# Kernel tuning notes

Hardware: AMD Instinct MI355X
Metric: run time of the kernel (lower is better)

Reference implementation:

```python
import jax, jax.numpy as jnp
import numpy as np
from jax import lax

T = 36          # sequence length
N_POLES = 80    # N -> dictionary has 2N+1 = 161 atoms
LAM = 0.1       # lam_f
MAX_ITER = 100
TOL = 1e-05


def real_D(T, rho, theta):
    # CONSTR=True: squash rho into [0.001, 1.15], theta into [0, pi]
    rmin, rmax = 0.001, 1.15
    r = rmin + (rmax - rmin) * jax.nn.sigmoid(rho)          # (N,)
    th = jnp.pi * jax.nn.sigmoid(theta)                     # (N,)
    i = jnp.arange(T, dtype=rho.dtype)[:, None]             # (T,1)
    p = r[None, :] ** i                                     # (T,N)
    W1 = p * jnp.cos(i * th[None, :])
    W2 = p * jnp.sin(i * th[None, :])
    D = jnp.concatenate([jnp.ones((T, 1), rho.dtype), W1, W2], axis=1)  # (T, 2N+1)
    # NORM=True: column-normalize all but the constant column
    norms = jnp.linalg.norm(D[:, 1:], axis=0, keepdims=True)
    return jnp.concatenate([D[:, :1], D[:, 1:] / norms], axis=1)


def softshrink(v, thr):
    return jnp.sign(v) * jnp.maximum(jnp.abs(v) - thr, 0.0)


def fista_efc(D, Y, lam, max_iter):
    # argmin_C ||Y - D C||_2^2 + lam |C|_1
    DtD = D.T @ D                                           # (P,P)
    L_inv = 1.0 / jnp.linalg.norm(DtD, ord=2)               # 1/spectral norm
    P = DtD.shape[0]
    dim_data = Y.shape[-1]
    A = jnp.eye(P, dtype=Y.dtype) - L_inv * DtD             # (P,P)
    B = L_inv * jnp.einsum('tp,btd->bpd', D, Y)             # (B,P,d)
    thr = lax.stop_gradient(lam * L_inv)                    # .item() in torch => constant

    batch = Y.shape[0]
    x0 = jnp.zeros((batch, P, dim_data), Y.dtype)
    y0 = jnp.zeros((batch, P, dim_data), Y.dtype)

    def body(carry, _):
        x, y, t, done = carry
        x_new = softshrink(jnp.einsum('pq,bqd->bpd', A, y) + B, thr)
        diff = jnp.linalg.norm(x - x_new) / dim_data        # Frobenius over all elems
        t_new = (1.0 + jnp.sqrt(1.0 + 4.0 * t * t)) / 2.0
        tt = (t - 1.0) / t_new
        y_new = (1.0 + tt) * x_new - tt * x
        # if already converged before this step, freeze the state (early return)
        x_out = jnp.where(done, x, x_new)
        y_out = jnp.where(done, y, y_new)
        t_out = jnp.where(done, t, t_new)
        done_new = done | (diff < TOL)
        return (x_out, y_out, t_out, done_new), None

    init = (x0, y0, jnp.float32(1.0), jnp.bool_(False))
    (x_fin, _, _, _), _ = lax.scan(body, init, None, length=max_iter)
    return x_fin


def reference(x, rho, theta):
    # DAN.forward with wiRH=False, freezeD=False
    dic = real_D(T, rho, theta)                             # (T, 2N+1)
    C = fista_efc(dic, x, LAM, MAX_ITER)                    # (B, 2N+1, d)
    reconst = jnp.einsum('tp,bpd->btd', dic, C)             # (B, T, d)
    return C, dic, reconst


def setup_inputs() -> dict:
    key = jax.random.key(0)
    k1, k2, k3 = jax.random.split(key, 3)
    x = jax.random.normal(k1, (256, T, 50), dtype=jnp.float32)
    rho = jax.random.uniform(k2, (N_POLES,), dtype=jnp.float32)
    theta = jax.random.uniform(k3, (N_POLES,), dtype=jnp.float32)
    return {"x": x, "rho": rho, "theta": theta}
```

## Files before the change

kernel.cpp:

```cpp
#include <hip/hip_runtime.h>
#include <math.h>

typedef _Float16 half_t;
typedef __attribute__((ext_vector_type(8))) _Float16 half8;
typedef __attribute__((ext_vector_type(4))) _Float16 half4;
typedef __attribute__((ext_vector_type(4))) float floatx4;

#define TDIM 36
#define PDIM 161
#define NCOL 50
#define NITER 100
#define PITER8 50

#define NKA 6
#define GSTR 44
#define SPS 196

#define YROW 384
#define RROW 128

#define SWZ(row, byteoff) ((byteoff) ^ (((row) & 7) << 4))

#define BY_Y    0
#define BY_R    24576
#define BY_LRTH 28672
#define BY_SC   32768
#define BY_GS   32784
#define BY_G2   39120
#define BY_G4   45456
#define LDS_TOTAL 51792

#define MFMA16 __builtin_amdgcn_mfma_f32_16x16x32_f16

__global__ __launch_bounds__(768, 3)
void dan_kernel(const float* __restrict__ xin, const float* __restrict__ rho,
                const float* __restrict__ theta, float* __restrict__ outC,
                float* __restrict__ outDic, float* __restrict__ outR)
{
  extern __shared__ char smc[];
  float*  sc   = (float*)(smc + BY_SC);
  float*  Gs   = (float*)(smc + BY_GS);
  float*  G2   = (float*)(smc + BY_G2);
  float*  G4   = (float*)(smc + BY_G4);
  float*  Df   = (float*)(smc + BY_Y);
  float*  lrth = (float*)(smc + BY_LRTH);

  const int tid = threadIdx.x;
  const int b = blockIdx.x;
  const int wave = tid >> 6, lane = tid & 63;
  const int q = lane >> 4, ln = lane & 15;

  {
    unsigned int* z = (unsigned int*)smc;
    for (int i = tid; i < LDS_TOTAL / 4; i += 768) z[i] = 0u;
  }
  __syncthreads();

  if (tid >= 1 && tid < PDIM) {
    const bool is_sin = tid > 80;
    const int n = is_sin ? (tid - 81) : (tid - 1);
    lrth[tid]       = logf(0.001f + 1.149f / (1.0f + expf(-rho[n])));
    lrth[161 + tid] = 3.14159265358979f / (1.0f + expf(-theta[n]));
  }
  __syncthreads();

  for (int i = tid; i < TDIM * PDIM; i += 768) {
    const int t = i / PDIM, p = i - t * PDIM;
    float val;
    if (p == 0) {
      val = 1.0f;
    } else {
      const float ft = (float)t;
      const float e = expf(ft * lrth[p]);
      const float ang = ft * lrth[161 + p];
      val = e * (p > 80 ? sinf(ang) : cosf(ang));
    }
    Df[t * SPS + p] = val;
  }
  __syncthreads();

  if (tid >= 1 && tid < PDIM) {
    float s2 = 0.0f;
    for (int t = 0; t < TDIM; ++t) {
      const float v = Df[t * SPS + tid];
      s2 += v * v;
    }
    const float inv = 1.0f / sqrtf(s2);
    for (int t = 0; t < TDIM; ++t) Df[t * SPS + tid] *= inv;
  }
  __syncthreads();

  if (tid < 666) {
    int i = 0, rem = tid;
    while (rem >= TDIM - i) { rem -= TDIM - i; ++i; }
    const int j = i + rem;
    const float4* ri = (const float4*)(Df + i * SPS);
    const float4* rj = (const float4*)(Df + j * SPS);
    float a = 0.0f;
    #pragma unroll 7
    for (int k = 0; k < SPS / 4; ++k) {
      const float4 x = ri[k], y = rj[k];
      a += x.x * y.x + x.y * y.y + x.z * y.z + x.w * y.w;
    }
    Gs[i * GSTR + j] = a;
    Gs[j * GSTR + i] = a;
  }
  if (b == 0) {
    for (int i = tid; i < TDIM * PDIM; i += 768) {
      const int t = i / PDIM, p = i - t * PDIM;
      outDic[i] = Df[t * SPS + p];
    }
  }

  const int mtA = wave >> 2;
  const int ntA = wave & 3;
  const int g = wave >> 1;
  const int h = wave & 1;

  half8 DhF[NKA], DlF[NKA];
  {
    const int row = 16 * mtA + ln;
    #pragma unroll
    for (int ks = 0; ks < NKA; ++ks) {
      half8 hh = {0,0,0,0,0,0,0,0}, ll = {0,0,0,0,0,0,0,0};
      if (row < TDIM) {
        const float4 f0 = *(const float4*)(Df + row * SPS + 32 * ks + 8 * q);
        const float4 f1 = *(const float4*)(Df + row * SPS + 32 * ks + 8 * q + 4);
        const float fa[8] = {f0.x, f0.y, f0.z, f0.w, f1.x, f1.y, f1.z, f1.w};
        #pragma unroll
        for (int e = 0; e < 8; ++e) {
          const half_t h2 = (half_t)fa[e];
          hh[e] = h2;
          ll[e] = (half_t)(fa[e] - (float)h2);
        }
      }
      DhF[ks] = hh;
      DlF[ks] = ll;
    }
  }
  half8 DtH[2][2];
  #pragma unroll
  for (int k = 0; k < 2; ++k) {
    const int atom = 16 * (g + 6 * k) + ln;
    #pragma unroll
    for (int ks = 0; ks < 2; ++ks) {
      half8 hh;
      #pragma unroll
      for (int e = 0; e < 8; ++e) {
        const int t = 32 * ks + 8 * q + e;
        const float v = (t < TDIM) ? Df[t * SPS + atom] : 0.0f;
        hh[e] = (half_t)v;
      }
      DtH[k][ks] = hh;
    }
  }
  float yA[4];
  {
    const float* xb = xin + b * TDIM * NCOL;
    const int c = 16 * ntA + ln;
    #pragma unroll
    for (int r = 0; r < 4; ++r) {
      const int t = 16 * mtA + 4 * q + r;
      yA[r] = (t < TDIM && c < NCOL) ? xb[t * NCOL + c] : 0.0f;
    }
  }
  __syncthreads();

  if (tid < 666) {
    int i = 0, rem = tid;
    while (rem >= TDIM - i) { rem -= TDIM - i; ++i; }
    const int j = i + rem;
    const float4* ri = (const float4*)(Gs + i * GSTR);
    const float4* rj = (const float4*)(Gs + j * GSTR);
    float a = 0.0f;
    #pragma unroll
    for (int k = 0; k < GSTR / 4; ++k) {
      const float4 x = ri[k], y = rj[k];
      a += x.x * y.x + x.y * y.y + x.z * y.z + x.w * y.w;
    }
    G2[i * GSTR + j] = a;
    G2[j * GSTR + i] = a;
  }
  __syncthreads();
  if (tid < 666) {
    int i = 0, rem = tid;
    while (rem >= TDIM - i) { rem -= TDIM - i; ++i; }
    const int j = i + rem;
    const float4* ri = (const float4*)(G2 + i * GSTR);
    const float4* rj = (const float4*)(G2 + j * GSTR);
    float a = 0.0f;
    #pragma unroll
    for (int k = 0; k < GSTR / 4; ++k) {
      const float4 x = ri[k], y = rj[k];
      a += x.x * y.x + x.y * y.y + x.z * y.z + x.w * y.w;
    }
    G4[i * GSTR + j] = a;
    G4[j * GSTR + i] = a;
  }
  __syncthreads();
  if (tid < 666) {
    int i = 0, rem = tid;
    while (rem >= TDIM - i) { rem -= TDIM - i; ++i; }
    const int j = i + rem;
    const float4* ri = (const float4*)(G4 + i * GSTR);
    const float4* rj = (const float4*)(G4 + j * GSTR);
    float a = 0.0f;
    #pragma unroll
    for (int k = 0; k < GSTR / 4; ++k) {
      const float4 x = ri[k], y = rj[k];
      a += x.x * y.x + x.y * y.y + x.z * y.z + x.w * y.w;
    }
    G2[i * GSTR + j] = a;
    G2[j * GSTR + i] = a;
  }
  __syncthreads();

  if (wave == 0) {
    float g8r[36];
    #pragma unroll
    for (int j = 0; j < 36; ++j) g8r[j] = (lane < 36) ? G2[lane * GSTR + j] : 0.0f;
    float v = (lane < 36) ? 1.0f : 0.0f;
    for (int it = 0; it < PITER8; ++it) {
      const int vi = __float_as_int(v);
      float w0 = 0.0f, w1 = 0.0f, w2 = 0.0f, w3 = 0.0f;
      #pragma unroll
      for (int j = 0; j < 36; j += 4) {
        w0 = fmaf(g8r[j],     __int_as_float(__builtin_amdgcn_readlane(vi, j)),     w0);
        w1 = fmaf(g8r[j + 1], __int_as_float(__builtin_amdgcn_readlane(vi, j + 1)), w1);
        w2 = fmaf(g8r[j + 2], __int_as_float(__builtin_amdgcn_readlane(vi, j + 2)), w2);
        w3 = fmaf(g8r[j + 3], __int_as_float(__builtin_amdgcn_readlane(vi, j + 3)), w3);
      }
      float w = (w0 + w1) + (w2 + w3);
      float s = w * w;
      #pragma unroll
      for (int off = 32; off > 0; off >>= 1) s += __shfl_xor(s, off, 64);
      v = w * rsqrtf(s);
    }
    const int vi = __float_as_int(v);
    float w0 = 0.0f, w1 = 0.0f;
    #pragma unroll
    for (int j = 0; j < 36; j += 2) {
      const float gi0 = (lane < 36) ? Gs[lane * GSTR + j]     : 0.0f;
      const float gi1 = (lane < 36) ? Gs[lane * GSTR + j + 1] : 0.0f;
      w0 = fmaf(gi0, __int_as_float(__builtin_amdgcn_readlane(vi, j)),     w0);
      w1 = fmaf(gi1, __int_as_float(__builtin_amdgcn_readlane(vi, j + 1)), w1);
    }
    float num = v * (w0 + w1);
    #pragma unroll
    for (int off = 32; off > 0; off >>= 1) num += __shfl_xor(num, off, 64);
    if (lane == 0) {
      sc[0] = 1.0f / num;
      sc[1] = 0.1f / num;
    }
  } else {
    unsigned int* z = (unsigned int*)smc;
    for (int i = tid - 64; i < 32768 / 4; i += 704) z[i] = 0u;
  }
  __syncthreads();
  const float L_inv = sc[0];
  const float thr = sc[1];

  float xR[2][2][4], yR[2][2][4];
  #pragma unroll
  for (int k = 0; k < 2; ++k)
    #pragma unroll
    for (int s = 0; s < 2; ++s)
      #pragma unroll
      for (int r = 0; r < 4; ++r) { xR[k][s][r] = 0.0f; yR[k][s][r] = 0.0f; }

  float tk = 1.0f;

  for (int it = 0; it < NITER; ++it) {
    {
      floatx4 aH0 = {0.f,0.f,0.f,0.f}, aH1 = {0.f,0.f,0.f,0.f};
      floatx4 aL0 = {0.f,0.f,0.f,0.f}, aL1 = {0.f,0.f,0.f,0.f};
      const int n0 = 16 * ntA + ln;
      const char* yrow = smc + BY_Y + n0 * YROW;
      #pragma unroll
      for (int ks = 0; ks < NKA; ++ks) {
        const int kb = (32 * ks + 8 * q) * 2;
        const half8 b0 = *(const half8*)(yrow + SWZ(n0, kb));
        if (ks & 1) {
          aH1 = MFMA16(DhF[ks], b0, aH1, 0, 0, 0);
          aL1 = MFMA16(DlF[ks], b0, aL1, 0, 0, 0);
        } else {
          aH0 = MFMA16(DhF[ks], b0, aH0, 0, 0, 0);
          aL0 = MFMA16(DlF[ks], b0, aL0, 0, 0, 0);
        }
      }
      const int t0 = 16 * mtA + 4 * q;
      half4 hv;
      #pragma unroll
      for (int r = 0; r < 4; ++r)
        hv[r] = (half_t)(yA[r] - ((aH0[r] + aH1[r]) + (aL0[r] + aL1[r])));
      *(half4*)(smc + BY_R + n0 * RROW + SWZ(n0, t0 * 2)) = hv;
    }
    __syncthreads();

    const float tnew = 0.5f * (1.0f + sqrtf(1.0f + 4.0f * tk * tk));
    const float ttf = (tk - 1.0f) / tnew;
    tk = tnew;

    {
      half8 rb[2][2];
      #pragma unroll
      for (int s = 0; s < 2; ++s) {
        const int cS = 16 * (2 * h + s) + ln;
        const char* rrow = smc + BY_R + cS * RROW;
        rb[s][0] = *(const half8*)(rrow + SWZ(cS, 16 * q));
        rb[s][1] = *(const half8*)(rrow + SWZ(cS, 64 + 16 * q));
      }

      #pragma unroll
      for (int k = 0; k < 2; ++k) {
        const int pt = g + 6 * k;
        const int p0 = 16 * pt + 4 * q;
        #pragma unroll
        for (int s = 0; s < 2; ++s) {
          floatx4 a = {0.f,0.f,0.f,0.f};
          a = MFMA16(DtH[k][0], rb[s][0], a, 0, 0, 0);
          a = MFMA16(DtH[k][1], rb[s][1], a, 0, 0, 0);
          const int cS = 16 * (2 * h + s) + ln;
          half4 hv;
          #pragma unroll
          for (int r = 0; r < 4; ++r) {
            const float w = yR[k][s][r] + L_inv * a[r];
            const float cl = fminf(fmaxf(w, -thr), thr);
            const float xn = w - cl;
            const float yn = xn + ttf * (xn - xR[k][s][r]);
            xR[k][s][r] = xn;
            yR[k][s][r] = yn;
            hv[r] = (half_t)yn;
          }
          *(half4*)(smc + BY_Y + cS * YROW + SWZ(cS, p0 * 2)) = hv;
        }
      }
    }
    __syncthreads();
  }

  float* Cb = outC + b * PDIM * NCOL;
  #pragma unroll
  for (int k = 0; k < 2; ++k) {
    const int pt = g + 6 * k;
    #pragma unroll
    for (int s = 0; s < 2; ++s) {
      const int cS = 16 * (2 * h + s) + ln;
      if (cS < NCOL) {
        #pragma unroll
        for (int r = 0; r < 4; ++r) {
          const int p = 16 * pt + 4 * q + r;
          if (p < PDIM) Cb[p * NCOL + cS] = xR[k][s][r];
        }
      }
    }
  }
  #pragma unroll
  for (int k = 0; k < 2; ++k) {
    const int pt = g + 6 * k;
    const int p0 = 16 * pt + 4 * q;
    #pragma unroll
    for (int s = 0; s < 2; ++s) {
      const int cS = 16 * (2 * h + s) + ln;
      half4 hv;
      #pragma unroll
      for (int r = 0; r < 4; ++r) hv[r] = (half_t)xR[k][s][r];
      *(half4*)(smc + BY_Y + cS * YROW + SWZ(cS, p0 * 2)) = hv;
    }
  }
  __syncthreads();
  {
    floatx4 aH0 = {0.f,0.f,0.f,0.f}, aH1 = {0.f,0.f,0.f,0.f};
    floatx4 aL0 = {0.f,0.f,0.f,0.f}, aL1 = {0.f,0.f,0.f,0.f};
    const int n0 = 16 * ntA + ln;
    const char* yrow = smc + BY_Y + n0 * YROW;
    #pragma unroll
    for (int ks = 0; ks < NKA; ++ks) {
      const int kb = (32 * ks + 8 * q) * 2;
      const half8 b0 = *(const half8*)(yrow + SWZ(n0, kb));
      if (ks & 1) {
        aH1 = MFMA16(DhF[ks], b0, aH1, 0, 0, 0);
        aL1 = MFMA16(DlF[ks], b0, aL1, 0, 0, 0);
      } else {
        aH0 = MFMA16(DhF[ks], b0, aH0, 0, 0, 0);
        aL0 = MFMA16(DlF[ks], b0, aL0, 0, 0, 0);
      }
    }
    float* Rb = outR + b * TDIM * NCOL;
    const int c = n0;
    if (c < NCOL) {
      const int t0 = 16 * mtA + 4 * q;
      #pragma unroll
      for (int r = 0; r < 4; ++r) {
        const int t = t0 + r;
        if (t < TDIM)
          Rb[t * NCOL + c] = (aH0[r] + aH1[r]) + (aL0[r] + aL1[r]);
      }
    }
  }
}


extern "C" void kernel_launch(void* const* d_in, const int* in_sizes, int n_in,
                              void* d_out, int out_size, void* d_ws, size_t ws_size,
                              hipStream_t stream) {
  const float* x     = (const float*)d_in[0];
  const float* rho   = (const float*)d_in[1];
  const float* theta = (const float*)d_in[2];

  float* out    = (float*)d_out;
  float* outC   = out;
  float* outDic = out + 256 * PDIM * NCOL;
  float* outR   = outDic + TDIM * PDIM;

  hipLaunchKernelGGL(dan_kernel, dim3(256), dim3(768), LDS_TOTAL, stream,
                     x, rho, theta, outC, outDic, outR);
}
```

Measured before the change: 210.9 us.

## Split each batch's 50 columns across two 384-thread blocks

Launches 512 blocks of 384 threads instead of 256 blocks of 768, with each block handling 25 of the 50 data columns of one batch element. The FISTA iterations are independent per column, so this halves per-block work and LDS use and gives more blocks to spread across CUs. The cost is that every block recomputes the dictionary, the Gram powers and the spectral-norm estimate. Column tiles stay 32 wide, so part of the MFMA work on 25 columns is padding.

```diff
diff --git a/kernel.cpp b/kernel.cpp
--- a/kernel.cpp
+++ b/kernel.cpp
@@ -9,6 +9,7 @@
 #define TDIM 36
 #define PDIM 161
 #define NCOL 50
+#define DHALF 25
 #define NITER 100
 #define PITER8 50
 
@@ -22,17 +23,18 @@
 #define SWZ(row, byteoff) ((byteoff) ^ (((row) & 7) << 4))
 
 #define BY_Y    0
-#define BY_R    24576
-#define BY_LRTH 28672
-#define BY_SC   32768
-#define BY_GS   32784
-#define BY_G2   39120
-#define BY_G4   45456
-#define LDS_TOTAL 51792
+#define BY_R    12288
+#define BY_DFX  16384
+#define BY_LRTH 28224
+#define BY_SC   29512
+#define BY_GS   29536
+#define BY_G2   35872
+#define BY_G4   42208
+#define LDS_TOTAL 48544
 
 #define MFMA16 __builtin_amdgcn_mfma_f32_16x16x32_f16
 
-__global__ __launch_bounds__(768, 3)
+__global__ __launch_bounds__(384, 4)
 void dan_kernel(const float* __restrict__ xin, const float* __restrict__ rho,
                 const float* __restrict__ theta, float* __restrict__ outC,
                 float* __restrict__ outDic, float* __restrict__ outR)
@@ -46,13 +48,15 @@
   float*  lrth = (float*)(smc + BY_LRTH);
 
   const int tid = threadIdx.x;
-  const int b = blockIdx.x;
+  const int blk = blockIdx.x;
+  const int b  = blk >> 1;
+  const int dh = blk & 1;
   const int wave = tid >> 6, lane = tid & 63;
   const int q = lane >> 4, ln = lane & 15;
 
   {
     unsigned int* z = (unsigned int*)smc;
-    for (int i = tid; i < LDS_TOTAL / 4; i += 768) z[i] = 0u;
+    for (int i = tid; i < LDS_TOTAL / 4; i += 384) z[i] = 0u;
   }
   __syncthreads();
 
@@ -64,7 +68,7 @@
   }
   __syncthreads();
 
-  for (int i = tid; i < TDIM * PDIM; i += 768) {
+  for (int i = tid; i < TDIM * PDIM; i += 384) {
     const int t = i / PDIM, p = i - t * PDIM;
     float val;
     if (p == 0) {
@@ -90,8 +94,8 @@
   }
   __syncthreads();
 
-  if (tid < 666) {
-    int i = 0, rem = tid;
+  for (int job = tid; job < 666; job += 384) {
+    int i = 0, rem = job;
     while (rem >= TDIM - i) { rem -= TDIM - i; ++i; }
     const int j = i + rem;
     const float4* ri = (const float4*)(Df + i * SPS);
@@ -105,17 +109,16 @@
     Gs[i * GSTR + j] = a;
     Gs[j * GSTR + i] = a;
   }
-  if (b == 0) {
-    for (int i = tid; i < TDIM * PDIM; i += 768) {
+  if (blk == 0) {
+    for (int i = tid; i < TDIM * PDIM; i += 384) {
       const int t = i / PDIM, p = i - t * PDIM;
       outDic[i] = Df[t * SPS + p];
     }
   }
 
-  const int mtA = wave >> 2;
-  const int ntA = wave & 3;
-  const int g = wave >> 1;
-  const int h = wave & 1;
+  const int mtA = wave >> 1;
+  const int ntA = wave & 1;
+  const int g = wave;
 
   half8 DhF[NKA], DlF[NKA];
   {
@@ -161,13 +164,13 @@
     #pragma unroll
     for (int r = 0; r < 4; ++r) {
       const int t = 16 * mtA + 4 * q + r;
-      yA[r] = (t < TDIM && c < NCOL) ? xb[t * NCOL + c] : 0.0f;
-    }
-  }
-  __syncthreads();
-
-  if (tid < 666) {
-    int i = 0, rem = tid;
+      yA[r] = (t < TDIM && c < DHALF) ? xb[t * NCOL + dh * DHALF + c] : 0.0f;
+    }
+  }
+  __syncthreads();
+
+  for (int job = tid; job < 666; job += 384) {
+    int i = 0, rem = job;
     while (rem >= TDIM - i) { rem -= TDIM - i; ++i; }
     const int j = i + rem;
     const float4* ri = (const float4*)(Gs + i * GSTR);
@@ -182,8 +185,8 @@
     G2[j * GSTR + i] = a;
   }
   __syncthreads();
-  if (tid < 666) {
-    int i = 0, rem = tid;
+  for (int job = tid; job < 666; job += 384) {
+    int i = 0, rem = job;
     while (rem >= TDIM - i) { rem -= TDIM - i; ++i; }
     const int j = i + rem;
     const float4* ri = (const float4*)(G2 + i * GSTR);
@@ -198,8 +201,8 @@
     G4[j * GSTR + i] = a;
   }
   __syncthreads();
-  if (tid < 666) {
-    int i = 0, rem = tid;
+  for (int job = tid; job < 666; job += 384) {
+    int i = 0, rem = job;
     while (rem >= TDIM - i) { rem -= TDIM - i; ++i; }
     const int j = i + rem;
     const float4* ri = (const float4*)(G4 + i * GSTR);
@@ -254,7 +257,7 @@
     }
   } else {
     unsigned int* z = (unsigned int*)smc;
-    for (int i = tid - 64; i < 32768 / 4; i += 704) z[i] = 0u;
+    for (int i = tid - 64; i < (BY_R + 4096) / 4; i += 320) z[i] = 0u;
   }
   __syncthreads();
   const float L_inv = sc[0];
@@ -305,7 +308,7 @@
       half8 rb[2][2];
       #pragma unroll
       for (int s = 0; s < 2; ++s) {
-        const int cS = 16 * (2 * h + s) + ln;
+        const int cS = 16 * s + ln;
         const char* rrow = smc + BY_R + cS * RROW;
         rb[s][0] = *(const half8*)(rrow + SWZ(cS, 16 * q));
         rb[s][1] = *(const half8*)(rrow + SWZ(cS, 64 + 16 * q));
@@ -320,7 +323,7 @@
           floatx4 a = {0.f,0.f,0.f,0.f};
           a = MFMA16(DtH[k][0], rb[s][0], a, 0, 0, 0);
           a = MFMA16(DtH[k][1], rb[s][1], a, 0, 0, 0);
-          const int cS = 16 * (2 * h + s) + ln;
+          const int cS = 16 * s + ln;
           half4 hv;
           #pragma unroll
           for (int r = 0; r < 4; ++r) {
@@ -339,14 +342,14 @@
     __syncthreads();
   }
 
-  float* Cb = outC + b * PDIM * NCOL;
+  float* Cb = outC + b * PDIM * NCOL + dh * DHALF;
   #pragma unroll
   for (int k = 0; k < 2; ++k) {
     const int pt = g + 6 * k;
     #pragma unroll
     for (int s = 0; s < 2; ++s) {
-      const int cS = 16 * (2 * h + s) + ln;
-      if (cS < NCOL) {
+      const int cS = 16 * s + ln;
+      if (cS < DHALF) {
         #pragma unroll
         for (int r = 0; r < 4; ++r) {
           const int p = 16 * pt + 4 * q + r;
@@ -361,7 +364,7 @@
     const int p0 = 16 * pt + 4 * q;
     #pragma unroll
     for (int s = 0; s < 2; ++s) {
-      const int cS = 16 * (2 * h + s) + ln;
+      const int cS = 16 * s + ln;
       half4 hv;
       #pragma unroll
       for (int r = 0; r < 4; ++r) hv[r] = (half_t)xR[k][s][r];
@@ -386,9 +389,9 @@
         aL0 = MFMA16(DlF[ks], b0, aL0, 0, 0, 0);
       }
     }
-    float* Rb = outR + b * TDIM * NCOL;
+    float* Rb = outR + b * TDIM * NCOL + dh * DHALF;
     const int c = n0;
-    if (c < NCOL) {
+    if (c < DHALF) {
       const int t0 = 16 * mtA + 4 * q;
       #pragma unroll
       for (int r = 0; r < 4; ++r) {
@@ -413,6 +416,6 @@
   float* outDic = out + 256 * PDIM * NCOL;
   float* outR   = outDic + TDIM * PDIM;
 
-  hipLaunchKernelGGL(dan_kernel, dim3(256), dim3(768), LDS_TOTAL, stream,
+  hipLaunchKernelGGL(dan_kernel, dim3(512), dim3(384), LDS_TOTAL, stream,
                      x, rho, theta, outC, outDic, outR);
 }
```

Result: slower. 287.1 us (+36.1%).

## Precompute negated Gram matrix in fp16 and run single-MFMA FISTA step with double-buffered Y

Applied to the files above, without the earlier changes.

Replaces the per-iteration two-stage residual update (D*y, then D^T*r) with one multiply by a precomputed -D^T D Gram matrix held in fp16 registers, plus a precomputed B = L_inv*D^T x bias. The Y buffer is double-buffered in LDS so each iteration needs only one barrier instead of two. The momentum coefficients are tabulated up front, and the final reconstruction drops the hi/lo fp16 split. This removes one matmul stage and one barrier per iteration, at the cost of much more LDS (about 149 KB, likely limiting occupancy to one block per CU) and lower precision, since both the Gram matrix and the final D are rounded to fp16.

```diff
diff --git a/kernel.cpp b/kernel.cpp
--- a/kernel.cpp
+++ b/kernel.cpp
@@ -14,21 +14,25 @@
 
 #define NKA 6
 #define GSTR 44
-#define SPS 196
+#define SPS 164
 
 #define YROW 384
-#define RROW 128
+#define GAR  384
+#define DROW 384
+#define TROW 128
 
 #define SWZ(row, byteoff) ((byteoff) ^ (((row) & 7) << 4))
 
 #define BY_Y    0
-#define BY_R    24576
-#define BY_LRTH 28672
-#define BY_SC   32768
-#define BY_GS   32784
-#define BY_G2   39120
-#define BY_G4   45456
-#define LDS_TOTAL 51792
+#define BY_GA   24576
+#define BY_DAH  98304
+#define BY_DT   112128
+#define BY_LRTH 134656
+#define BY_SC   135944
+#define BY_TTF  135960
+#define BY_GS   136360
+#define BY_G8   142696
+#define LDS_TOTAL 149032
 
 #define MFMA16 __builtin_amdgcn_mfma_f32_16x16x32_f16
 
@@ -39,9 +43,11 @@
 {
   extern __shared__ char smc[];
   float*  sc   = (float*)(smc + BY_SC);
+  float*  ttfT = (float*)(smc + BY_TTF);
   float*  Gs   = (float*)(smc + BY_GS);
-  float*  G2   = (float*)(smc + BY_G2);
-  float*  G4   = (float*)(smc + BY_G4);
+  float*  G2a  = (float*)(smc + BY_GA);
+  float*  G4a  = (float*)(smc + BY_GA + 6336);
+  float*  G8p  = (float*)(smc + BY_G8);
   float*  Df   = (float*)(smc + BY_Y);
   float*  lrth = (float*)(smc + BY_LRTH);
 
@@ -97,7 +103,6 @@
     const float4* ri = (const float4*)(Df + i * SPS);
     const float4* rj = (const float4*)(Df + j * SPS);
     float a = 0.0f;
-    #pragma unroll 7
     for (int k = 0; k < SPS / 4; ++k) {
       const float4 x = ri[k], y = rj[k];
       a += x.x * y.x + x.y * y.y + x.z * y.z + x.w * y.w;
@@ -105,64 +110,13 @@
     Gs[i * GSTR + j] = a;
     Gs[j * GSTR + i] = a;
   }
-  if (b == 0) {
-    for (int i = tid; i < TDIM * PDIM; i += 768) {
-      const int t = i / PDIM, p = i - t * PDIM;
-      outDic[i] = Df[t * SPS + p];
-    }
-  }
-
-  const int mtA = wave >> 2;
-  const int ntA = wave & 3;
-  const int g = wave >> 1;
-  const int h = wave & 1;
-
-  half8 DhF[NKA], DlF[NKA];
-  {
-    const int row = 16 * mtA + ln;
-    #pragma unroll
-    for (int ks = 0; ks < NKA; ++ks) {
-      half8 hh = {0,0,0,0,0,0,0,0}, ll = {0,0,0,0,0,0,0,0};
-      if (row < TDIM) {
-        const float4 f0 = *(const float4*)(Df + row * SPS + 32 * ks + 8 * q);
-        const float4 f1 = *(const float4*)(Df + row * SPS + 32 * ks + 8 * q + 4);
-        const float fa[8] = {f0.x, f0.y, f0.z, f0.w, f1.x, f1.y, f1.z, f1.w};
-        #pragma unroll
-        for (int e = 0; e < 8; ++e) {
-          const half_t h2 = (half_t)fa[e];
-          hh[e] = h2;
-          ll[e] = (half_t)(fa[e] - (float)h2);
-        }
-      }
-      DhF[ks] = hh;
-      DlF[ks] = ll;
-    }
-  }
-  half8 DtH[2][2];
-  #pragma unroll
-  for (int k = 0; k < 2; ++k) {
-    const int atom = 16 * (g + 6 * k) + ln;
-    #pragma unroll
-    for (int ks = 0; ks < 2; ++ks) {
-      half8 hh;
-      #pragma unroll
-      for (int e = 0; e < 8; ++e) {
-        const int t = 32 * ks + 8 * q + e;
-        const float v = (t < TDIM) ? Df[t * SPS + atom] : 0.0f;
-        hh[e] = (half_t)v;
-      }
-      DtH[k][ks] = hh;
-    }
-  }
-  float yA[4];
-  {
-    const float* xb = xin + b * TDIM * NCOL;
-    const int c = 16 * ntA + ln;
-    #pragma unroll
-    for (int r = 0; r < 4; ++r) {
-      const int t = 16 * mtA + 4 * q + r;
-      yA[r] = (t < TDIM && c < NCOL) ? xb[t * NCOL + c] : 0.0f;
-    }
+  for (int i = tid; i < TDIM * PDIM; i += 768) {
+    const int t = i / PDIM, p = i - t * PDIM;
+    const float v = Df[t * SPS + p];
+    const half_t hh = (half_t)v;
+    *(half_t*)(smc + BY_DT + p * TROW + SWZ(p, t * 2)) = hh;
+    *(half_t*)(smc + BY_DAH + t * DROW + SWZ(t, p * 2)) = hh;
+    if (b == 0) outDic[i] = v;
   }
   __syncthreads();
 
@@ -178,47 +132,47 @@
       const float4 x = ri[k], y = rj[k];
       a += x.x * y.x + x.y * y.y + x.z * y.z + x.w * y.w;
     }
-    G2[i * GSTR + j] = a;
-    G2[j * GSTR + i] = a;
+    G2a[i * GSTR + j] = a;
+    G2a[j * GSTR + i] = a;
   }
   __syncthreads();
   if (tid < 666) {
     int i = 0, rem = tid;
     while (rem >= TDIM - i) { rem -= TDIM - i; ++i; }
     const int j = i + rem;
-    const float4* ri = (const float4*)(G2 + i * GSTR);
-    const float4* rj = (const float4*)(G2 + j * GSTR);
+    const float4* ri = (const float4*)(G2a + i * GSTR);
+    const float4* rj = (const float4*)(G2a + j * GSTR);
     float a = 0.0f;
     #pragma unroll
     for (int k = 0; k < GSTR / 4; ++k) {
       const float4 x = ri[k], y = rj[k];
       a += x.x * y.x + x.y * y.y + x.z * y.z + x.w * y.w;
     }
-    G4[i * GSTR + j] = a;
-    G4[j * GSTR + i] = a;
+    G4a[i * GSTR + j] = a;
+    G4a[j * GSTR + i] = a;
   }
   __syncthreads();
   if (tid < 666) {
     int i = 0, rem = tid;
     while (rem >= TDIM - i) { rem -= TDIM - i; ++i; }
     const int j = i + rem;
-    const float4* ri = (const float4*)(G4 + i * GSTR);
-    const float4* rj = (const float4*)(G4 + j * GSTR);
+    const float4* ri = (const float4*)(G4a + i * GSTR);
+    const float4* rj = (const float4*)(G4a + j * GSTR);
     float a = 0.0f;
     #pragma unroll
     for (int k = 0; k < GSTR / 4; ++k) {
       const float4 x = ri[k], y = rj[k];
       a += x.x * y.x + x.y * y.y + x.z * y.z + x.w * y.w;
     }
-    G2[i * GSTR + j] = a;
-    G2[j * GSTR + i] = a;
+    G8p[i * GSTR + j] = a;
+    G8p[j * GSTR + i] = a;
   }
   __syncthreads();
 
   if (wave == 0) {
     float g8r[36];
     #pragma unroll
-    for (int j = 0; j < 36; ++j) g8r[j] = (lane < 36) ? G2[lane * GSTR + j] : 0.0f;
+    for (int j = 0; j < 36; ++j) g8r[j] = (lane < 36) ? G8p[lane * GSTR + j] : 0.0f;
     float v = (lane < 36) ? 1.0f : 0.0f;
     for (int it = 0; it < PITER8; ++it) {
       const int vi = __float_as_int(v);
@@ -253,12 +207,99 @@
       sc[1] = 0.1f / num;
     }
   } else {
-    unsigned int* z = (unsigned int*)smc;
-    for (int i = tid - 64; i < 32768 / 4; i += 704) z[i] = 0u;
+    for (int i = tid - 64; i < 33 * 16; i += 704) {
+      const int row = i >> 4, hh = i & 15;
+      *(half_t*)(smc + BY_GA + row * GAR + SWZ(row, (176 + hh) * 2)) = (half_t)0.0f;
+    }
+    for (int tile = wave - 1; tile < 121; tile += 11) {
+      const int pti = tile / 11, ntj = tile - 11 * (tile / 11);
+      const int rowA = 16 * pti + ln, rowB = 16 * ntj + ln;
+      const char* da = smc + BY_DT + rowA * TROW;
+      const char* db = smc + BY_DT + rowB * TROW;
+      const half8 a0 = *(const half8*)(da + SWZ(rowA, 16 * q));
+      const half8 a1 = *(const half8*)(da + SWZ(rowA, 64 + 16 * q));
+      const half8 b0 = *(const half8*)(db + SWZ(rowB, 16 * q));
+      const half8 b1 = *(const half8*)(db + SWZ(rowB, 64 + 16 * q));
+      floatx4 acc = {0.f, 0.f, 0.f, 0.f};
+      acc = MFMA16(a0, b0, acc, 0, 0, 0);
+      acc = MFMA16(a1, b1, acc, 0, 0, 0);
+      const int gcol = 16 * ntj + ln;
+      #pragma unroll
+      for (int r = 0; r < 4; ++r) {
+        const int gi = 16 * pti + 4 * q + r;
+        *(half_t*)(smc + BY_GA + gi * GAR + SWZ(gi, gcol * 2)) = (half_t)(-acc[r]);
+      }
+    }
+    if (tid == 64) {
+      float t = 1.0f;
+      for (int it = 0; it < NITER; ++it) {
+        const float tn = 0.5f * (1.0f + sqrtf(1.0f + 4.0f * t * t));
+        ttfT[it] = (t - 1.0f) / tn;
+        t = tn;
+      }
+    }
   }
   __syncthreads();
   const float L_inv = sc[0];
   const float thr = sc[1];
+
+  const int g = wave >> 1;
+  const int h = wave & 1;
+
+  half8 GF[2][NKA];
+  #pragma unroll
+  for (int k = 0; k < 2; ++k) {
+    const int row = 16 * (g + 6 * k) + ln;
+    const char* ga = smc + BY_GA + row * GAR;
+    #pragma unroll
+    for (int ks = 0; ks < NKA; ++ks)
+      GF[k][ks] = *(const half8*)(ga + SWZ(row, (32 * ks + 8 * q) * 2));
+  }
+  float Bc[2][2][4];
+  {
+    const float* xb = xin + b * TDIM * NCOL;
+    #pragma unroll
+    for (int k = 0; k < 2; ++k) {
+      #pragma unroll
+      for (int s = 0; s < 2; ++s) {
+        const int cS = 16 * (2 * h + s) + ln;
+        #pragma unroll
+        for (int r = 0; r < 4; ++r) {
+          const int p = 16 * (g + 6 * k) + 4 * q + r;
+          float acc = 0.0f;
+          if (p < PDIM && cS < NCOL) {
+            for (int t = 0; t < TDIM; ++t)
+              acc = fmaf(Df[t * SPS + p], xb[t * NCOL + cS], acc);
+          }
+          Bc[k][s][r] = L_inv * acc;
+        }
+      }
+    }
+  }
+  __syncthreads();
+  {
+    unsigned int* z = (unsigned int*)smc;
+    for (int i = tid; i < 24576 / 4; i += 768) {
+      z[i] = 0u;
+      z[i + 24576 / 4] = 0u;
+    }
+  }
+  __syncthreads();
+
+  const char* yrd[2][NKA];
+  char* ywr[2][2];
+  #pragma unroll
+  for (int s = 0; s < 2; ++s) {
+    const int cS = 16 * (2 * h + s) + ln;
+    #pragma unroll
+    for (int ks = 0; ks < NKA; ++ks)
+      yrd[s][ks] = smc + BY_Y + cS * YROW + SWZ(cS, (32 * ks + 8 * q) * 2);
+    #pragma unroll
+    for (int k = 0; k < 2; ++k) {
+      const int p0 = 16 * (g + 6 * k) + 4 * q;
+      ywr[k][s] = smc + BY_Y + cS * YROW + SWZ(cS, p0 * 2);
+    }
+  }
 
   float xR[2][2][4], yR[2][2][4];
   #pragma unroll
@@ -268,74 +309,41 @@
       #pragma unroll
       for (int r = 0; r < 4; ++r) { xR[k][s][r] = 0.0f; yR[k][s][r] = 0.0f; }
 
-  float tk = 1.0f;
-
-  for (int it = 0; it < NITER; ++it) {
-    {
-      floatx4 aH0 = {0.f,0.f,0.f,0.f}, aH1 = {0.f,0.f,0.f,0.f};
-      floatx4 aL0 = {0.f,0.f,0.f,0.f}, aL1 = {0.f,0.f,0.f,0.f};
-      const int n0 = 16 * ntA + ln;
-      const char* yrow = smc + BY_Y + n0 * YROW;
-      #pragma unroll
-      for (int ks = 0; ks < NKA; ++ks) {
-        const int kb = (32 * ks + 8 * q) * 2;
-        const half8 b0 = *(const half8*)(yrow + SWZ(n0, kb));
-        if (ks & 1) {
-          aH1 = MFMA16(DhF[ks], b0, aH1, 0, 0, 0);
-          aL1 = MFMA16(DlF[ks], b0, aL1, 0, 0, 0);
-        } else {
-          aH0 = MFMA16(DhF[ks], b0, aH0, 0, 0, 0);
-          aL0 = MFMA16(DlF[ks], b0, aL0, 0, 0, 0);
-        }
-      }
-      const int t0 = 16 * mtA + 4 * q;
-      half4 hv;
-      #pragma unroll
-      for (int r = 0; r < 4; ++r)
-        hv[r] = (half_t)(yA[r] - ((aH0[r] + aH1[r]) + (aL0[r] + aL1[r])));
-      *(half4*)(smc + BY_R + n0 * RROW + SWZ(n0, t0 * 2)) = hv;
-    }
+#define ITER_BODY(RD, WR, ITIDX)                                               \
+  do {                                                                         \
+    const float ttf = ttfT[ITIDX];                                             \
+    _Pragma("unroll")                                                          \
+    for (int s = 0; s < 2; ++s) {                                              \
+      half8 yb[NKA];                                                           \
+      _Pragma("unroll")                                                        \
+      for (int ks = 0; ks < NKA; ++ks)                                         \
+        yb[ks] = *(const half8*)(yrd[s][ks] + (RD));                           \
+      _Pragma("unroll")                                                        \
+      for (int k = 0; k < 2; ++k) {                                            \
+        floatx4 a = {0.f, 0.f, 0.f, 0.f};                                      \
+        _Pragma("unroll")                                                      \
+        for (int ks = 0; ks < NKA; ++ks)                                       \
+          a = MFMA16(GF[k][ks], yb[ks], a, 0, 0, 0);                           \
+        half4 hv;                                                              \
+        _Pragma("unroll")                                                      \
+        for (int r = 0; r < 4; ++r) {                                          \
+          const float w = yR[k][s][r] + fmaf(L_inv, a[r], Bc[k][s][r]);        \
+          const float cl = fminf(fmaxf(w, -thr), thr);                         \
+          const float xn = w - cl;                                             \
+          const float yn = xn + ttf * (xn - xR[k][s][r]);                      \
+          xR[k][s][r] = xn;                                                    \
+          yR[k][s][r] = yn;                                                    \
+          hv[r] = (half_t)yn;                                                  \
+        }                                                                      \
+        *(half4*)(ywr[k][s] + (WR)) = hv;                                      \
+      }                                                                        \
+    }                                                                          \
+  } while (0)
+
+  for (int it = 0; it < NITER; it += 2) {
+    ITER_BODY(0, 24576, it);
     __syncthreads();
-
-    const float tnew = 0.5f * (1.0f + sqrtf(1.0f + 4.0f * tk * tk));
-    const float ttf = (tk - 1.0f) / tnew;
-    tk = tnew;
-
-    {
-      half8 rb[2][2];
-      #pragma unroll
-      for (int s = 0; s < 2; ++s) {
-        const int cS = 16 * (2 * h + s) + ln;
-        const char* rrow = smc + BY_R + cS * RROW;
-        rb[s][0] = *(const half8*)(rrow + SWZ(cS, 16 * q));
-        rb[s][1] = *(const half8*)(rrow + SWZ(cS, 64 + 16 * q));
-      }
-
-      #pragma unroll
-      for (int k = 0; k < 2; ++k) {
-        const int pt = g + 6 * k;
-        const int p0 = 16 * pt + 4 * q;
-        #pragma unroll
-        for (int s = 0; s < 2; ++s) {
-          floatx4 a = {0.f,0.f,0.f,0.f};
-          a = MFMA16(DtH[k][0], rb[s][0], a, 0, 0, 0);
-          a = MFMA16(DtH[k][1], rb[s][1], a, 0, 0, 0);
-          const int cS = 16 * (2 * h + s) + ln;
-          half4 hv;
-          #pragma unroll
-          for (int r = 0; r < 4; ++r) {
-            const float w = yR[k][s][r] + L_inv * a[r];
-            const float cl = fminf(fmaxf(w, -thr), thr);
-            const float xn = w - cl;
-            const float yn = xn + ttf * (xn - xR[k][s][r]);
-            xR[k][s][r] = xn;
-            yR[k][s][r] = yn;
-            hv[r] = (half_t)yn;
-          }
-          *(half4*)(smc + BY_Y + cS * YROW + SWZ(cS, p0 * 2)) = hv;
-        }
-      }
-    }
+    ITER_BODY(24576, 0, it + 1);
     __syncthreads();
   }
 
@@ -357,44 +365,36 @@
   }
   #pragma unroll
   for (int k = 0; k < 2; ++k) {
-    const int pt = g + 6 * k;
-    const int p0 = 16 * pt + 4 * q;
     #pragma unroll
     for (int s = 0; s < 2; ++s) {
-      const int cS = 16 * (2 * h + s) + ln;
       half4 hv;
       #pragma unroll
       for (int r = 0; r < 4; ++r) hv[r] = (half_t)xR[k][s][r];
-      *(half4*)(smc + BY_Y + cS * YROW + SWZ(cS, p0 * 2)) = hv;
+      *(half4*)(ywr[k][s]) = hv;
     }
   }
   __syncthreads();
   {
-    floatx4 aH0 = {0.f,0.f,0.f,0.f}, aH1 = {0.f,0.f,0.f,0.f};
-    floatx4 aL0 = {0.f,0.f,0.f,0.f}, aL1 = {0.f,0.f,0.f,0.f};
+    const int mtA = wave >> 2, ntA = wave & 3;
+    const int rowD = 16 * mtA + ln;
     const int n0 = 16 * ntA + ln;
-    const char* yrow = smc + BY_Y + n0 * YROW;
+    const half8 zz = {0, 0, 0, 0, 0, 0, 0, 0};
+    floatx4 a = {0.f, 0.f, 0.f, 0.f};
     #pragma unroll
     for (int ks = 0; ks < NKA; ++ks) {
-      const int kb = (32 * ks + 8 * q) * 2;
-      const half8 b0 = *(const half8*)(yrow + SWZ(n0, kb));
-      if (ks & 1) {
-        aH1 = MFMA16(DhF[ks], b0, aH1, 0, 0, 0);
-        aL1 = MFMA16(DlF[ks], b0, aL1, 0, 0, 0);
-      } else {
-        aH0 = MFMA16(DhF[ks], b0, aH0, 0, 0, 0);
-        aL0 = MFMA16(DlF[ks], b0, aL0, 0, 0, 0);
-      }
+      const half8 dh_ = (rowD < TDIM)
+        ? *(const half8*)(smc + BY_DAH + rowD * DROW + SWZ(rowD, (32 * ks + 8 * q) * 2))
+        : zz;
+      const half8 yb = *(const half8*)(smc + BY_Y + n0 * YROW + SWZ(n0, (32 * ks + 8 * q) * 2));
+      a = MFMA16(dh_, yb, a, 0, 0, 0);
     }
     float* Rb = outR + b * TDIM * NCOL;
-    const int c = n0;
-    if (c < NCOL) {
+    if (n0 < NCOL) {
       const int t0 = 16 * mtA + 4 * q;
       #pragma unroll
       for (int r = 0; r < 4; ++r) {
         const int t = t0 + r;
-        if (t < TDIM)
-          Rb[t * NCOL + c] = (aH0[r] + aH1[r]) + (aL0[r] + aL1[r]);
+        if (t < TDIM) Rb[t * NCOL + n0] = a[r];
       }
     }
   }
```

After: 261.1 us. 1.24x slower.
